# Kernel tuning notes

Measured on AMD Instinct MI355X. Metric: run time of the kernel, lower is better.

Reference implementation:

```python
import jax, jax.numpy as jnp
import numpy as np

N = 1_000_000   # total nodes (variable + check)
V = 600_000     # variable nodes (mask = first V nodes)
H = 128         # hidden_dim


def setup_inputs() -> dict:
    key = jax.random.key(0)
    k0, k1, k2, k3 = jax.random.split(key, 4)
    node_features = jax.random.normal(k0, (N, H), dtype=jnp.float32)
    original_llr = jax.random.normal(k1, (V,), dtype=jnp.float32)
    # canonical layout: variable nodes occupy the first V slots
    var_node_mask = jnp.arange(N) < V
    # llr_proj: Linear(1, H)
    W_llr = jax.random.normal(k2, (1, H), dtype=jnp.float32) * 0.1
    b_llr = jnp.zeros((H,), dtype=jnp.float32)
    # gate: Linear(2H, H) followed by sigmoid
    W_gate = jax.random.normal(k3, (2 * H, H), dtype=jnp.float32) * (1.0 / np.sqrt(2 * H))
    b_gate = jnp.zeros((H,), dtype=jnp.float32)
    return {
        "node_features": node_features,
        "original_llr": original_llr,
        "W_llr": W_llr,
        "b_llr": b_llr,
        "W_gate": W_gate,
        "b_gate": b_gate,
        "var_node_mask": var_node_mask,
    }


def reference(node_features, original_llr, W_llr, b_llr, W_gate, b_gate, var_node_mask):
    # var_node_mask is, by construction, True exactly for the first V nodes,
    # so the masked gather/scatter reduces to static slicing (jit-friendly).
    num_var = original_llr.shape[0]
    var_features = node_features[:num_var]                      # [V, H] gather
    # Linear(1 -> H): outer product of scalar llr with weight row + bias
    llr_features = original_llr[:, None] * W_llr[0] + b_llr      # [V, H]
    gate_in = jnp.concatenate([var_features, llr_features], axis=-1)  # [V, 2H]
    gate = jax.nn.sigmoid(gate_in @ W_gate + b_gate)             # [V, H]
    fused = gate * llr_features + (1.0 - gate) * var_features    # convex combo
    return node_features.at[:num_var].set(fused)                 # scatter back
```

## Files before the change

### kernel.cpp

```cpp
#include <hip/hip_runtime.h>
#include <hip/hip_bf16.h>

constexpr int H = 128;
constexpr int V = 600000;
constexpr int NTOT = 1000000;

typedef short bf16x8 __attribute__((ext_vector_type(8)));
typedef float f32x4 __attribute__((ext_vector_type(4)));
typedef unsigned int u32;

__device__ __forceinline__ short f2bf(float f) {
    unsigned u = __float_as_uint(f);
    u += 0x7FFF + ((u >> 16) & 1);
    return (short)(u >> 16);
}

__device__ __forceinline__ void async_copy16(char* ldsDst, const float* gSrc) {
    __builtin_amdgcn_global_load_lds(
        (const __attribute__((address_space(1))) u32*)gSrc,
        (__attribute__((address_space(3))) u32*)ldsDst, 16, 0, 0);
}

__global__ void precompute_uc_kernel(const float* __restrict__ W_llr,
                                     const float* __restrict__ b_llr,
                                     const float* __restrict__ W_gate,
                                     const float* __restrict__ b_gate,
                                     float* __restrict__ uc) {
    int h = threadIdx.x;
    float u = 0.0f, c = 0.0f;
    for (int k = 0; k < H; ++k) {
        float w2 = W_gate[(size_t)(H + k) * H + h];
        u += W_llr[k] * w2;
        c += b_llr[k] * w2;
    }
    uc[h] = u;
    uc[H + h] = c + b_gate[h];
    uc[2 * H + h] = W_llr[h];
    uc[3 * H + h] = b_llr[h];
}

#define LDS_BYTES 32768
#define ABUF 16384

__global__ __launch_bounds__(256, 4) void fused_residual_llr_kernel(
    const float* __restrict__ nf,
    const float* __restrict__ llr,
    const float* __restrict__ W_gate,
    const float* __restrict__ uc,
    float* __restrict__ out) {
    int b = blockIdx.x;
    int tid = threadIdx.x;

    if ((b & 3) == 3) {
        size_t base = (size_t)V * H;
        const float4* src = reinterpret_cast<const float4*>(nf + base);
        float4* dst = reinterpret_cast<float4*>(out + base);
        size_t i0 = (size_t)(b >> 2) * 256 + tid;
        const size_t stride = 250u * 256u;
#pragma unroll 1
        for (int s = 0; s < 50; ++s) {
            size_t i = i0 + (size_t)s * (stride * 4);
            float4 v0 = src[i];
            float4 v1 = src[i + stride];
            float4 v2 = src[i + 2 * stride];
            float4 v3 = src[i + 3 * stride];
            dst[i] = v0;
            dst[i + stride] = v1;
            dst[i + 2 * stride] = v2;
            dst[i + 3 * stride] = v3;
        }
        return;
    }
    int cb = (b >> 2) * 3 + (b & 3);

    __shared__ __align__(16) char lds[LDS_BYTES];

    int lane = tid & 63;
    int w = tid >> 6;
    int l15 = lane & 15;
    int l4 = lane >> 4;

#pragma unroll 4
    for (int j = 0; j < 16; ++j) {
        int idx = tid + 256 * j;
        int k = idx >> 5, c4 = idx & 31;
        float4 wv = reinterpret_cast<const float4*>(W_gate)[(size_t)k * 32 + c4];
        float wa[4] = {wv.x, wv.y, wv.z, wv.w};
#pragma unroll
        for (int e = 0; e < 4; ++e) {
            int n = c4 * 4 + e;
            *reinterpret_cast<short*>(lds + n * 256 + k * 2) = f2bf(wa[e]);
        }
    }
    float u_r[2], c_r[2], wl_r[2], bl_r[2];
#pragma unroll
    for (int nfr = 0; nfr < 2; ++nfr) {
        int col = w * 32 + nfr * 16 + l15;
        u_r[nfr]  = uc[col];
        c_r[nfr]  = uc[128 + col];
        wl_r[nfr] = uc[256 + col];
        bl_r[nfr] = uc[384 + col];
    }
    __syncthreads();

    bf16x8 Bf[4][2];
#pragma unroll
    for (int kk = 0; kk < 4; ++kk)
#pragma unroll
        for (int nfr = 0; nfr < 2; ++nfr) {
            int n = w * 32 + nfr * 16 + l15;
            Bf[kk][nfr] = *reinterpret_cast<const bf16x8*>(
                lds + n * 256 + kk * 64 + l4 * 16);
        }
    __syncthreads();

    int rowBase0 = cb * 800;

#pragma unroll
    for (int j = 0; j < 4; ++j) {
        int rl = (w * 4 + j) * 2 + (lane >> 5);
        int gg = (lane & 31) ^ (rl & 7);
        async_copy16(lds + (w * 4 + j) * 1024,
                     nf + (size_t)(rowBase0 + rl) * H + gg * 4);
    }

    int cur = 0;
#pragma unroll 1
    for (int t = 0; t < 25; ++t) {
        int rowBase = rowBase0 + t * 32;
        __syncthreads();

        if (t < 24) {
            char* nbuf = lds + (cur ^ 1) * ABUF;
            int rowN = rowBase + 32;
#pragma unroll
            for (int j = 0; j < 4; ++j) {
                int rl = (w * 4 + j) * 2 + (lane >> 5);
                int gg = (lane & 31) ^ (rl & 7);
                async_copy16(nbuf + (w * 4 + j) * 1024,
                             nf + (size_t)(rowN + rl) * H + gg * 4);
            }
        }
        float llr_r[8];
#pragma unroll
        for (int rg = 0; rg < 2; ++rg)
#pragma unroll
            for (int reg = 0; reg < 4; ++reg)
                llr_r[rg * 4 + reg] = llr[rowBase + rg * 16 + l4 * 4 + reg];

        char* buf = lds + cur * ABUF;
        f32x4 acc[2][2];
#pragma unroll
        for (int rg = 0; rg < 2; ++rg)
#pragma unroll
            for (int nfr = 0; nfr < 2; ++nfr)
                acc[rg][nfr] = (f32x4){0.f, 0.f, 0.f, 0.f};

#pragma unroll
        for (int kk = 0; kk < 4; ++kk) {
#pragma unroll
            for (int rg = 0; rg < 2; ++rg) {
                int rl = rg * 16 + l15;
                int g0 = (l4 * 2) ^ (l15 & 7);
                const char* base = buf + rl * 512 + kk * 128;
                f32x4 lo = *reinterpret_cast<const f32x4*>(base + (g0 << 4));
                f32x4 hi = *reinterpret_cast<const f32x4*>(base + ((g0 ^ 1) << 4));
                bf16x8 a;
                a[0] = f2bf(lo[0]); a[1] = f2bf(lo[1]);
                a[2] = f2bf(lo[2]); a[3] = f2bf(lo[3]);
                a[4] = f2bf(hi[0]); a[5] = f2bf(hi[1]);
                a[6] = f2bf(hi[2]); a[7] = f2bf(hi[3]);
                acc[rg][0] = __builtin_amdgcn_mfma_f32_16x16x32_bf16(
                    a, Bf[kk][0], acc[rg][0], 0, 0, 0);
                acc[rg][1] = __builtin_amdgcn_mfma_f32_16x16x32_bf16(
                    a, Bf[kk][1], acc[rg][1], 0, 0, 0);
            }
        }

#pragma unroll
        for (int rg = 0; rg < 2; ++rg) {
#pragma unroll
            for (int reg = 0; reg < 4; ++reg) {
                int rl = rg * 16 + l4 * 4 + reg;
                float lr = llr_r[rg * 4 + reg];
#pragma unroll
                for (int nfr = 0; nfr < 2; ++nfr) {
                    int col = w * 32 + nfr * 16 + l15;
                    float x = acc[rg][nfr][reg] + fmaf(lr, u_r[nfr], c_r[nfr]);
                    float g = 1.0f / (1.0f + __expf(-x));
                    int gcol = w * 8 + nfr * 4 + (l15 >> 2);
                    float vf = *reinterpret_cast<const float*>(
                        buf + rl * 512 + ((gcol ^ (rl & 7)) << 4) + (l15 & 3) * 4);
                    float lf = fmaf(lr, wl_r[nfr], bl_r[nfr]);
                    out[(size_t)(rowBase + rl) * H + col] = fmaf(g, lf - vf, vf);
                }
            }
        }
        cur ^= 1;
    }
}

extern "C" void kernel_launch(void* const* d_in, const int* in_sizes, int n_in,
                              void* d_out, int out_size, void* d_ws, size_t ws_size,
                              hipStream_t stream) {
    const float* nf     = (const float*)d_in[0];
    const float* llr    = (const float*)d_in[1];
    const float* W_llr  = (const float*)d_in[2];
    const float* b_llr  = (const float*)d_in[3];
    const float* W_gate = (const float*)d_in[4];
    const float* b_gate = (const float*)d_in[5];
    float* out = (float*)d_out;
    float* uc  = (float*)d_ws;

    precompute_uc_kernel<<<1, 128, 0, stream>>>(W_llr, b_llr, W_gate, b_gate, uc);

    fused_residual_llr_kernel<<<1000, 256, 0, stream>>>(nf, llr, W_gate, uc, out);
}
```

Before: 246.4 us.

## Triple-buffer 16-row tiles with async LLR staging and vmcnt-based waits

Shrinks each tile from 32 to 16 rows and adds a three-stage LDS ring buffer that prefetches two tiles ahead. LLR values are now staged into LDS with async 4-byte copies instead of being loaded per thread from global memory. The single __syncthreads is replaced by explicit s_waitcnt vmcnt counts plus s_barrier. The aim is deeper memory-latency hiding in this bandwidth-bound kernel. The hand-counted vmcnt values are fragile: the global stores also count toward vmcnt, and the STAGE macro's issue count has to match the waits exactly.

```diff
diff --git a/kernel.cpp b/kernel.cpp
--- a/kernel.cpp
+++ b/kernel.cpp
@@ -4,6 +4,7 @@
 constexpr int H = 128;
 constexpr int V = 600000;
 constexpr int NTOT = 1000000;
+constexpr int NT = 50;
 
 typedef short bf16x8 __attribute__((ext_vector_type(8)));
 typedef float f32x4 __attribute__((ext_vector_type(4)));
@@ -20,6 +21,12 @@
         (const __attribute__((address_space(1))) u32*)gSrc,
         (__attribute__((address_space(3))) u32*)ldsDst, 16, 0, 0);
 }
+__device__ __forceinline__ void async_copy4(char* ldsDst, const float* gSrc) {
+    __builtin_amdgcn_global_load_lds(
+        (const __attribute__((address_space(1))) u32*)gSrc,
+        (__attribute__((address_space(3))) u32*)ldsDst, 4, 0, 0);
+}
+#define FENCE() asm volatile("" ::: "memory")
 
 __global__ void precompute_uc_kernel(const float* __restrict__ W_llr,
                                      const float* __restrict__ b_llr,
@@ -40,7 +47,8 @@
 }
 
 #define LDS_BYTES 32768
-#define ABUF 16384
+#define ABUF 8192
+#define LLR_BASE 24576
 
 __global__ __launch_bounds__(256, 4) void fused_residual_llr_kernel(
     const float* __restrict__ nf,
@@ -114,89 +122,84 @@
         }
     __syncthreads();
 
-    int rowBase0 = cb * 800;
-
-#pragma unroll
-    for (int j = 0; j < 4; ++j) {
-        int rl = (w * 4 + j) * 2 + (lane >> 5);
-        int gg = (lane & 31) ^ (rl & 7);
-        async_copy16(lds + (w * 4 + j) * 1024,
-                     nf + (size_t)(rowBase0 + rl) * H + gg * 4);
-    }
+    int rowBase0 = cb * (NT * 16);
+
+#define STAGE(tt, bi)                                                        \
+    {                                                                        \
+        char* nbuf_ = lds + (bi) * ABUF;                                     \
+        int rb_ = rowBase0 + (tt) * 16;                                      \
+        _Pragma("unroll")                                                    \
+        for (int j_ = 0; j_ < 2; ++j_) {                                     \
+            int seg_ = w * 2 + j_;                                           \
+            int rl_ = seg_ * 2 + (lane >> 5);                                \
+            int gg_ = (lane & 31) ^ (rl_ & 7);                               \
+            async_copy16(nbuf_ + seg_ * 1024,                                \
+                         nf + (size_t)(rb_ + rl_) * H + gg_ * 4);            \
+        }                                                                    \
+        async_copy4(lds + LLR_BASE + (bi) * 256, llr + rb_ + (lane & 15));   \
+    }
+
+    STAGE(0, 0);
+    FENCE();
+    STAGE(1, 1);
+    FENCE();
 
     int cur = 0;
 #pragma unroll 1
-    for (int t = 0; t < 25; ++t) {
-        int rowBase = rowBase0 + t * 32;
-        __syncthreads();
-
-        if (t < 24) {
-            char* nbuf = lds + (cur ^ 1) * ABUF;
-            int rowN = rowBase + 32;
-#pragma unroll
-            for (int j = 0; j < 4; ++j) {
-                int rl = (w * 4 + j) * 2 + (lane >> 5);
-                int gg = (lane & 31) ^ (rl & 7);
-                async_copy16(nbuf + (w * 4 + j) * 1024,
-                             nf + (size_t)(rowN + rl) * H + gg * 4);
+    for (int t = 0; t < NT; ++t) {
+        int rowBase = rowBase0 + t * 16;
+
+        if (t == NT - 1) asm volatile("s_waitcnt vmcnt(0)" ::: "memory");
+        else             asm volatile("s_waitcnt vmcnt(3)" ::: "memory");
+        __builtin_amdgcn_s_barrier();
+        FENCE();
+
+        if (t + 2 < NT) {
+            int tgt = (cur == 0) ? 2 : cur - 1;
+            STAGE(t + 2, tgt);
+        }
+        FENCE();
+
+        char* buf = lds + cur * ABUF;
+        f32x4 acc[2];
+        acc[0] = (f32x4){0.f, 0.f, 0.f, 0.f};
+        acc[1] = (f32x4){0.f, 0.f, 0.f, 0.f};
+#pragma unroll
+        for (int kk = 0; kk < 4; ++kk) {
+            int g0 = (l4 * 2) ^ (l15 & 7);
+            const char* base = buf + l15 * 512 + kk * 128;
+            f32x4 lo = *reinterpret_cast<const f32x4*>(base + (g0 << 4));
+            f32x4 hi = *reinterpret_cast<const f32x4*>(base + ((g0 ^ 1) << 4));
+            bf16x8 a;
+            a[0] = f2bf(lo[0]); a[1] = f2bf(lo[1]);
+            a[2] = f2bf(lo[2]); a[3] = f2bf(lo[3]);
+            a[4] = f2bf(hi[0]); a[5] = f2bf(hi[1]);
+            a[6] = f2bf(hi[2]); a[7] = f2bf(hi[3]);
+            acc[0] = __builtin_amdgcn_mfma_f32_16x16x32_bf16(
+                a, Bf[kk][0], acc[0], 0, 0, 0);
+            acc[1] = __builtin_amdgcn_mfma_f32_16x16x32_bf16(
+                a, Bf[kk][1], acc[1], 0, 0, 0);
+        }
+
+        const float* llrs = reinterpret_cast<const float*>(lds + LLR_BASE + cur * 256);
+#pragma unroll
+        for (int reg = 0; reg < 4; ++reg) {
+            int rl = l4 * 4 + reg;
+            float lr = llrs[rl];
+#pragma unroll
+            for (int nfr = 0; nfr < 2; ++nfr) {
+                int col = w * 32 + nfr * 16 + l15;
+                float x = acc[nfr][reg] + fmaf(lr, u_r[nfr], c_r[nfr]);
+                float g = 1.0f / (1.0f + __expf(-x));
+                int gcol = w * 8 + nfr * 4 + (l15 >> 2);
+                float vf = *reinterpret_cast<const float*>(
+                    buf + rl * 512 + ((gcol ^ (rl & 7)) << 4) + (l15 & 3) * 4);
+                float lf = fmaf(lr, wl_r[nfr], bl_r[nfr]);
+                out[(size_t)(rowBase + rl) * H + col] = fmaf(g, lf - vf, vf);
             }
         }
-        float llr_r[8];
-#pragma unroll
-        for (int rg = 0; rg < 2; ++rg)
-#pragma unroll
-            for (int reg = 0; reg < 4; ++reg)
-                llr_r[rg * 4 + reg] = llr[rowBase + rg * 16 + l4 * 4 + reg];
-
-        char* buf = lds + cur * ABUF;
-        f32x4 acc[2][2];
-#pragma unroll
-        for (int rg = 0; rg < 2; ++rg)
-#pragma unroll
-            for (int nfr = 0; nfr < 2; ++nfr)
-                acc[rg][nfr] = (f32x4){0.f, 0.f, 0.f, 0.f};
-
-#pragma unroll
-        for (int kk = 0; kk < 4; ++kk) {
-#pragma unroll
-            for (int rg = 0; rg < 2; ++rg) {
-                int rl = rg * 16 + l15;
-                int g0 = (l4 * 2) ^ (l15 & 7);
-                const char* base = buf + rl * 512 + kk * 128;
-                f32x4 lo = *reinterpret_cast<const f32x4*>(base + (g0 << 4));
-                f32x4 hi = *reinterpret_cast<const f32x4*>(base + ((g0 ^ 1) << 4));
-                bf16x8 a;
-                a[0] = f2bf(lo[0]); a[1] = f2bf(lo[1]);
-                a[2] = f2bf(lo[2]); a[3] = f2bf(lo[3]);
-                a[4] = f2bf(hi[0]); a[5] = f2bf(hi[1]);
-                a[6] = f2bf(hi[2]); a[7] = f2bf(hi[3]);
-                acc[rg][0] = __builtin_amdgcn_mfma_f32_16x16x32_bf16(
-                    a, Bf[kk][0], acc[rg][0], 0, 0, 0);
-                acc[rg][1] = __builtin_amdgcn_mfma_f32_16x16x32_bf16(
-                    a, Bf[kk][1], acc[rg][1], 0, 0, 0);
-            }
-        }
-
-#pragma unroll
-        for (int rg = 0; rg < 2; ++rg) {
-#pragma unroll
-            for (int reg = 0; reg < 4; ++reg) {
-                int rl = rg * 16 + l4 * 4 + reg;
-                float lr = llr_r[rg * 4 + reg];
-#pragma unroll
-                for (int nfr = 0; nfr < 2; ++nfr) {
-                    int col = w * 32 + nfr * 16 + l15;
-                    float x = acc[rg][nfr][reg] + fmaf(lr, u_r[nfr], c_r[nfr]);
-                    float g = 1.0f / (1.0f + __expf(-x));
-                    int gcol = w * 8 + nfr * 4 + (l15 >> 2);
-                    float vf = *reinterpret_cast<const float*>(
-                        buf + rl * 512 + ((gcol ^ (rl & 7)) << 4) + (l15 & 3) * 4);
-                    float lf = fmaf(lr, wl_r[nfr], bl_r[nfr]);
-                    out[(size_t)(rowBase + rl) * H + col] = fmaf(g, lf - vf, vf);
-                }
-            }
-        }
-        cur ^= 1;
+        FENCE();
+        cur = (cur == 2) ? 0 : cur + 1;
     }
 }
 
```

New measurement: 247.5 us. No clear change (+0.4%).
